# Performance work log

Hardware: AMD Instinct MI355X
Metric: run time of the kernel (lower is better)

## Reference

```python
import jax, jax.numpy as jnp
import numpy as np

N = 100000   # atoms (nodes)
M = 1600000  # bonds (edges)
D = 64       # atom_fea_len


def setup_inputs() -> dict:
    key = jax.random.key(0)
    ks = jax.random.split(key, 8)
    atom_weights = jax.random.uniform(ks[0], (N, 1), dtype=jnp.float32)
    atom_in_fea = jax.random.normal(ks[1], (N, D), dtype=jnp.float32)
    self_fea_idx = jnp.sort(jax.random.randint(ks[2], (M,), 0, N))
    nbr_fea_idx = jax.random.randint(ks[3], (M,), 0, N)
    # message_nn: Linear(2D->D) + LeakyReLU + Linear(D->D)
    W1 = jax.random.normal(ks[4], (2 * D, D), dtype=jnp.float32) * (1.0 / np.sqrt(2 * D))
    b1 = jnp.zeros((D,), dtype=jnp.float32)
    W2 = jax.random.normal(ks[5], (D, D), dtype=jnp.float32) * (1.0 / np.sqrt(D))
    b2 = jnp.zeros((D,), dtype=jnp.float32)
    # pool_nn (gate): Linear(D->1)
    Wg = jax.random.normal(ks[6], (D, 1), dtype=jnp.float32) * (1.0 / np.sqrt(D))
    bg = jnp.zeros((1,), dtype=jnp.float32)
    return {"atom_weights": atom_weights, "atom_in_fea": atom_in_fea,
            "self_fea_idx": self_fea_idx, "nbr_fea_idx": nbr_fea_idx,
            "W1": W1, "b1": b1, "W2": W2, "b2": b2, "Wg": Wg, "bg": bg}


def reference(atom_weights, atom_in_fea, self_fea_idx, nbr_fea_idx,
              W1, b1, W2, b2, Wg, bg):
    n = atom_in_fea.shape[0]
    # gather-concat: [M, 2D]
    fea = jnp.concatenate([atom_in_fea[self_fea_idx], atom_in_fea[nbr_fea_idx]], axis=1)
    # message_nn MLP -> [M, D]
    fea = jax.nn.leaky_relu(fea @ W1 + b1) @ W2 + b2
    # weighted scatter-softmax attention pooling over segments self_fea_idx
    gate = fea @ Wg + bg                                    # [M, 1]
    gmax = jax.ops.segment_max(gate, self_fea_idx, num_segments=n)  # [N, 1]
    gate = jnp.exp(gate - gmax[self_fea_idx])
    gate = atom_weights[nbr_fea_idx] * gate                 # [M, 1]
    denom = jax.ops.segment_sum(gate, self_fea_idx, num_segments=n)  # [N, 1]
    gate = gate / (denom[self_fea_idx] + 1e-13)
    pooled = jax.ops.segment_sum(gate * fea, self_fea_idx, num_segments=n)  # [N, D]
    return pooled + atom_in_fea
```

## Files before the change

### kernel.cpp

```cpp
#include <hip/hip_runtime.h>
#include <math.h>

typedef float f32x4 __attribute__((ext_vector_type(4)));
typedef __bf16 bf16x8 __attribute__((ext_vector_type(8)));

__global__ void build_row_start(const int* __restrict__ self_idx,
                                int* __restrict__ row_start, int M, int N) {
  int i = blockIdx.x * blockDim.x + threadIdx.x;
  if (i >= M) return;
  int cur = self_idx[i];
  int prev = (i == 0) ? -1 : self_idx[i - 1];
  for (int j = prev + 1; j <= cur; ++j) row_start[j] = i;
  if (i == M - 1) {
    for (int j = cur + 1; j <= N; ++j) row_start[j] = M;
  }
}

__global__ __launch_bounds__(256, 2)
void precompute_uy(const float* __restrict__ atom_fea,
                   const float* __restrict__ W1,
                   const float* __restrict__ b1,
                   const float* __restrict__ W2,
                   __bf16* __restrict__ Ub, __bf16* __restrict__ Yb,
                   __bf16* __restrict__ W2pack, int N) {
  const int lane = threadIdx.x & 63;
  const int r16 = lane & 15, g = lane >> 4;
  const int wid = (blockIdx.x * blockDim.x + threadIdx.x) >> 6;
  const int nw = (gridDim.x * blockDim.x) >> 6;

  if (wid == 0) {
#pragma unroll
    for (int ks = 0; ks < 2; ++ks)
#pragma unroll
      for (int c = 0; c < 4; ++c) {
        bf16x8 t;
#pragma unroll
        for (int jj = 0; jj < 8; ++jj)
          t[jj] = (__bf16)W2[(size_t)(32 * ks + 8 * g + jj) * 64 + 16 * c + r16];
        *(bf16x8*)(W2pack + ((size_t)(ks * 4 + c) * 64 + lane) * 8) = t;
      }
  }

  bf16x8 wt[2][4], wb[2][4];
#pragma unroll
  for (int ks = 0; ks < 2; ++ks)
#pragma unroll
    for (int c = 0; c < 4; ++c) {
      bf16x8 t, b;
#pragma unroll
      for (int jj = 0; jj < 8; ++jj) {
        int k = 32 * ks + 8 * g + jj;
        t[jj] = (__bf16)W1[(size_t)k * 64 + 16 * c + r16];
        b[jj] = (__bf16)W1[(size_t)(64 + k) * 64 + 16 * c + r16];
      }
      wt[ks][c] = t; wb[ks][c] = b;
    }
  float b1c[4];
#pragma unroll
  for (int c = 0; c < 4; ++c) b1c[c] = b1[16 * c + r16];

  const int nTiles = (N + 15) >> 4;
  for (int tile = wid; tile < nTiles; tile += nw) {
    const int a0 = tile * 16;
    int arow = a0 + r16; if (arow >= N) arow = N - 1;

    bf16x8 af[2];
#pragma unroll
    for (int ks = 0; ks < 2; ++ks) {
      const float* p = atom_fea + (size_t)arow * 64 + 32 * ks + 8 * g;
      f32x4 x0 = *(const f32x4*)p;
      f32x4 x1 = *(const f32x4*)(p + 4);
      bf16x8 a;
#pragma unroll
      for (int jj = 0; jj < 4; ++jj) { a[jj] = (__bf16)x0[jj]; a[4 + jj] = (__bf16)x1[jj]; }
      af[ks] = a;
    }

    f32x4 uacc[4], yacc[4];
#pragma unroll
    for (int c = 0; c < 4; ++c) { uacc[c] = (f32x4)0.0f; yacc[c] = (f32x4)0.0f; }
#pragma unroll
    for (int ks = 0; ks < 2; ++ks)
#pragma unroll
      for (int c = 0; c < 4; ++c) {
        uacc[c] = __builtin_amdgcn_mfma_f32_16x16x32_bf16(af[ks], wt[ks][c], uacc[c], 0, 0, 0);
        yacc[c] = __builtin_amdgcn_mfma_f32_16x16x32_bf16(af[ks], wb[ks][c], yacc[c], 0, 0, 0);
      }

#pragma unroll
    for (int c = 0; c < 4; ++c)
#pragma unroll
      for (int j = 0; j < 4; ++j) {
        int row = a0 + 4 * g + j;
        if (row < N) {
          Ub[(size_t)row * 64 + 16 * c + r16] = (__bf16)(uacc[c][j] + b1c[c]);
          Yb[(size_t)row * 64 + 16 * c + r16] = (__bf16)yacc[c][j];
        }
      }
  }
}

__global__ __launch_bounds__(64, 4)
void fused_pool(const float* __restrict__ atom_w,
                const float* __restrict__ atom_fea,
                const int* __restrict__ nbr_idx,
                const float* __restrict__ W2,
                const float* __restrict__ b2,
                const float* __restrict__ Wg,
                const float* __restrict__ bg,
                const int* __restrict__ row_start,
                const __bf16* __restrict__ Ub,
                const __bf16* __restrict__ Yb,
                const __bf16* __restrict__ W2pack,
                float* __restrict__ out, int N) {
  const int lane = threadIdx.x & 63;
  const int r16 = lane & 15, g = lane >> 4;
  const int wid = blockIdx.x;
  const int nw = gridDim.x;

  float wgl = 0.f;
  {
    const float* w2row = W2 + (size_t)lane * 64;
#pragma unroll
    for (int d = 0; d < 64; ++d) wgl = fmaf(w2row[d], Wg[d], wgl);
  }
  float wgsl[16];
#pragma unroll
  for (int ks = 0; ks < 2; ++ks)
#pragma unroll
    for (int jj = 0; jj < 8; ++jj)
      wgsl[ks * 8 + jj] = __shfl(wgl, 32 * ks + 8 * g + jj);

  float tb = b2[lane] * Wg[lane];
#pragma unroll
  for (int off = 1; off < 64; off <<= 1) tb += __shfl_xor(tb, off);
  const float bgp = bg[0] + tb;
  const float b2l = b2[lane];

  int s = wid;
  int nStart = 0, nEnd = 0;
  bf16x8 nu0 = {}, nu1 = {};
  if (s < N) {
    nStart = row_start[s];
    nEnd = row_start[s + 1];
    nu0 = *(const bf16x8*)(Ub + (size_t)s * 64 + 8 * g);
    nu1 = *(const bf16x8*)(Ub + (size_t)s * 64 + 32 + 8 * g);
  }

  for (; s < N; s += nw) {
    const int start = nStart, end = nEnd;
    const bf16x8 u0 = nu0, u1 = nu1;
    const float xr = atom_fea[(size_t)s * 64 + lane];

    const int s2 = s + nw;
    if (s2 < N) {
      nStart = row_start[s2];
      nEnd = row_start[s2 + 1];
      nu0 = *(const bf16x8*)(Ub + (size_t)s2 * 64 + 8 * g);
      nu1 = *(const bf16x8*)(Ub + (size_t)s2 * 64 + 32 + 8 * g);
    }

    float uf[16];
#pragma unroll
    for (int jj = 0; jj < 8; ++jj) {
      uf[jj] = (float)u0[jj];
      uf[8 + jj] = (float)u1[jj];
    }

    float zacc[16];
#pragma unroll
    for (int k = 0; k < 16; ++k) zacc[k] = 0.f;
    float wsum = 0.f;

    for (int base = start; base < end; base += 16) {
      const int er = base + r16;
      const bool valid = er < end;
      const int nb = valid ? nbr_idx[er] : 0;
      const float aw = atom_w[nb];
      const __bf16* yrow = Yb + ((size_t)nb << 6);
      const bf16x8 y0 = *(const bf16x8*)(yrow + 8 * g);
      const bf16x8 y1 = *(const bf16x8*)(yrow + 32 + 8 * g);

      float hf[16];
#pragma unroll
      for (int jj = 0; jj < 8; ++jj) {
        float a = uf[jj] + (float)y0[jj];
        float b = uf[8 + jj] + (float)y1[jj];
        hf[jj] = fmaxf(a, 0.01f * a);
        hf[8 + jj] = fmaxf(b, 0.01f * b);
      }

      float p0 = 0.f, p1 = 0.f;
#pragma unroll
      for (int i = 0; i < 8; ++i) {
        p0 = fmaf(hf[i], wgsl[i], p0);
        p1 = fmaf(hf[8 + i], wgsl[8 + i], p1);
      }
      float p = p0 + p1;
      p += __shfl_xor(p, 16);
      p += __shfl_xor(p, 32);

      const float w = valid ? aw * __expf(p + bgp) : 0.f;
      wsum += w;
#pragma unroll
      for (int k = 0; k < 16; ++k) zacc[k] = fmaf(w, hf[k], zacc[k]);
    }

    bf16x8 zf0, zf1;
#pragma unroll
    for (int jj = 0; jj < 8; ++jj) {
      zf0[jj] = (__bf16)zacc[jj];
      zf1[jj] = (__bf16)zacc[8 + jj];
    }

    f32x4 facc[4];
#pragma unroll
    for (int c = 0; c < 4; ++c) facc[c] = (f32x4)0.0f;
#pragma unroll
    for (int c = 0; c < 4; ++c) {
      const bf16x8 wf0 = *(const bf16x8*)(W2pack + ((size_t)(0 * 4 + c) * 64 + lane) * 8);
      const bf16x8 wf1 = *(const bf16x8*)(W2pack + ((size_t)(1 * 4 + c) * 64 + lane) * 8);
      facc[c] = __builtin_amdgcn_mfma_f32_16x16x32_bf16(zf0, wf0, facc[c], 0, 0, 0);
      facc[c] = __builtin_amdgcn_mfma_f32_16x16x32_bf16(zf1, wf1, facc[c], 0, 0, 0);
    }

    float accv[4];
#pragma unroll
    for (int c = 0; c < 4; ++c) {
      float a = (facc[c][0] + facc[c][1]) + (facc[c][2] + facc[c][3]);
      a += __shfl_xor(a, 16);
      a += __shfl_xor(a, 32);
      accv[c] = a;
    }

    float ssum = wsum;
    ssum += __shfl_xor(ssum, 1);
    ssum += __shfl_xor(ssum, 2);
    ssum += __shfl_xor(ssum, 4);
    ssum += __shfl_xor(ssum, 8);

    float val = accv[0];
    val = (g == 1) ? accv[1] : val;
    val = (g == 2) ? accv[2] : val;
    val = (g == 3) ? accv[3] : val;
    val = fmaf(ssum, b2l, val);

    out[(size_t)s * 64 + lane] = val / (ssum + 1e-13f) + xr;
  }
}

extern "C" void kernel_launch(void* const* d_in, const int* in_sizes, int n_in,
                              void* d_out, int out_size, void* d_ws, size_t ws_size,
                              hipStream_t stream) {
  const float* atom_w   = (const float*)d_in[0];
  const float* atom_fea = (const float*)d_in[1];
  const int*   self_idx = (const int*)d_in[2];
  const int*   nbr_idx  = (const int*)d_in[3];
  const float* W1 = (const float*)d_in[4];
  const float* b1 = (const float*)d_in[5];
  const float* W2 = (const float*)d_in[6];
  const float* b2 = (const float*)d_in[7];
  const float* Wg = (const float*)d_in[8];
  const float* bg = (const float*)d_in[9];
  float* out = (float*)d_out;

  const int N = in_sizes[0];
  const int M = in_sizes[2];

  char* ws = (char*)d_ws;
  int* row_start = (int*)ws;
  size_t off = ((size_t)(N + 1) * sizeof(int) + 255) & ~(size_t)255;
  __bf16* W2pack = (__bf16*)(ws + off);
  __bf16* Ub = W2pack + 8 * 64 * 8;
  __bf16* Yb = Ub + (size_t)N * 64;

  hipLaunchKernelGGL(build_row_start, dim3((M + 255) / 256), dim3(256), 0,
                     stream, self_idx, row_start, M, N);
  hipLaunchKernelGGL(precompute_uy, dim3(512), dim3(256), 0, stream,
                     atom_fea, W1, b1, W2, Ub, Yb, W2pack, N);
  hipLaunchKernelGGL(fused_pool, dim3(8192), dim3(64), 0, stream,
                     atom_w, atom_fea, nbr_idx, W2, b2, Wg, bg,
                     row_start, Ub, Yb, W2pack, out, N);
}
```

Baseline: 107.5 us.

## Process two atoms per wave with interleaved edge gathers in fused_pool

Each wave in the fused pooling kernel now handles a pair of consecutive atoms, issuing the neighbor gathers for both atoms before computing either one. The aim is more independent memory requests in flight per wave to hide gather latency, and to amortize the W2 MFMA epilogue over two atoms. The cross-iteration prefetch of row_start and U is removed, and launch bounds drop from 4 to 3 to make room for the extra registers. That lowers occupancy, and pairs with unequal degree leave one half idle.

Result: slower. 122.2 us (+13.7%).

```diff
diff --git a/kernel.cpp b/kernel.cpp
--- a/kernel.cpp
+++ b/kernel.cpp
@@ -100,7 +100,7 @@
   }
 }
 
-__global__ __launch_bounds__(64, 4)
+__global__ __launch_bounds__(64, 3)
 void fused_pool(const float* __restrict__ atom_w,
                 const float* __restrict__ atom_fea,
                 const int* __restrict__ nbr_idx,
@@ -115,8 +115,6 @@
                 float* __restrict__ out, int N) {
   const int lane = threadIdx.x & 63;
   const int r16 = lane & 15, g = lane >> 4;
-  const int wid = blockIdx.x;
-  const int nw = gridDim.x;
 
   float wgl = 0.f;
   {
@@ -137,115 +135,158 @@
   const float bgp = bg[0] + tb;
   const float b2l = b2[lane];
 
-  int s = wid;
-  int nStart = 0, nEnd = 0;
-  bf16x8 nu0 = {}, nu1 = {};
-  if (s < N) {
-    nStart = row_start[s];
-    nEnd = row_start[s + 1];
-    nu0 = *(const bf16x8*)(Ub + (size_t)s * 64 + 8 * g);
-    nu1 = *(const bf16x8*)(Ub + (size_t)s * 64 + 32 + 8 * g);
-  }
-
-  for (; s < N; s += nw) {
-    const int start = nStart, end = nEnd;
-    const bf16x8 u0 = nu0, u1 = nu1;
-    const float xr = atom_fea[(size_t)s * 64 + lane];
-
-    const int s2 = s + nw;
-    if (s2 < N) {
-      nStart = row_start[s2];
-      nEnd = row_start[s2 + 1];
-      nu0 = *(const bf16x8*)(Ub + (size_t)s2 * 64 + 8 * g);
-      nu1 = *(const bf16x8*)(Ub + (size_t)s2 * 64 + 32 + 8 * g);
-    }
-
-    float uf[16];
+  const int pstride = 2 * gridDim.x;
+  for (int p0 = 2 * blockIdx.x; p0 < N; p0 += pstride) {
+    const int sA = p0;
+    const int sB = p0 + 1;
+    const bool hasB = sB < N;
+
+    const int startA = row_start[sA];
+    const int endA = row_start[sA + 1];
+    const int startB = hasB ? row_start[sB] : 0;
+    const int endB = hasB ? row_start[sB + 1] : 0;
+
+    float ufA[16], ufB[16];
+    {
+      const bf16x8 a0 = *(const bf16x8*)(Ub + (size_t)sA * 64 + 8 * g);
+      const bf16x8 a1 = *(const bf16x8*)(Ub + (size_t)sA * 64 + 32 + 8 * g);
+      const bf16x8 c0 = hasB ? *(const bf16x8*)(Ub + (size_t)sB * 64 + 8 * g) : a0;
+      const bf16x8 c1 = hasB ? *(const bf16x8*)(Ub + (size_t)sB * 64 + 32 + 8 * g) : a1;
+#pragma unroll
+      for (int jj = 0; jj < 8; ++jj) {
+        ufA[jj] = (float)a0[jj]; ufA[8 + jj] = (float)a1[jj];
+        ufB[jj] = (float)c0[jj]; ufB[8 + jj] = (float)c1[jj];
+      }
+    }
+
+    float zA[16], zB[16];
+#pragma unroll
+    for (int k = 0; k < 16; ++k) { zA[k] = 0.f; zB[k] = 0.f; }
+    float wsumA = 0.f, wsumB = 0.f;
+
+    const int nTA = (endA - startA + 15) >> 4;
+    const int nTB = (endB - startB + 15) >> 4;
+    const int nT = nTA > nTB ? nTA : nTB;
+
+    for (int t = 0; t < nT; ++t) {
+      const int baseA = startA + 16 * t;
+      const int baseB = startB + 16 * t;
+      const bool actA = baseA < endA;
+      const bool actB = hasB && baseB < endB;
+
+      int nbA = 0; bf16x8 yA0 = {}, yA1 = {}; float awA = 0.f; bool vA = false;
+      int nbB = 0; bf16x8 yB0 = {}, yB1 = {}; float awB = 0.f; bool vB = false;
+      if (actA) {
+        const int e = baseA + r16; vA = e < endA;
+        nbA = vA ? nbr_idx[e] : 0;
+        const __bf16* yr = Yb + ((size_t)nbA << 6);
+        yA0 = *(const bf16x8*)(yr + 8 * g);
+        yA1 = *(const bf16x8*)(yr + 32 + 8 * g);
+        awA = atom_w[nbA];
+      }
+      if (actB) {
+        const int e = baseB + r16; vB = e < endB;
+        nbB = vB ? nbr_idx[e] : 0;
+        const __bf16* yr = Yb + ((size_t)nbB << 6);
+        yB0 = *(const bf16x8*)(yr + 8 * g);
+        yB1 = *(const bf16x8*)(yr + 32 + 8 * g);
+        awB = atom_w[nbB];
+      }
+
+      if (actA) {
+        float hf[16];
+#pragma unroll
+        for (int jj = 0; jj < 8; ++jj) {
+          float a = ufA[jj] + (float)yA0[jj];
+          float b = ufA[8 + jj] + (float)yA1[jj];
+          hf[jj] = fmaxf(a, 0.01f * a);
+          hf[8 + jj] = fmaxf(b, 0.01f * b);
+        }
+        float pacc = 0.f;
+#pragma unroll
+        for (int i = 0; i < 16; ++i) pacc = fmaf(hf[i], wgsl[i], pacc);
+        pacc += __shfl_xor(pacc, 16);
+        pacc += __shfl_xor(pacc, 32);
+        const float w = vA ? awA * __expf(pacc + bgp) : 0.f;
+        wsumA += w;
+#pragma unroll
+        for (int k = 0; k < 16; ++k) zA[k] = fmaf(w, hf[k], zA[k]);
+      }
+      if (actB) {
+        float hf[16];
+#pragma unroll
+        for (int jj = 0; jj < 8; ++jj) {
+          float a = ufB[jj] + (float)yB0[jj];
+          float b = ufB[8 + jj] + (float)yB1[jj];
+          hf[jj] = fmaxf(a, 0.01f * a);
+          hf[8 + jj] = fmaxf(b, 0.01f * b);
+        }
+        float pacc = 0.f;
+#pragma unroll
+        for (int i = 0; i < 16; ++i) pacc = fmaf(hf[i], wgsl[i], pacc);
+        pacc += __shfl_xor(pacc, 16);
+        pacc += __shfl_xor(pacc, 32);
+        const float w = vB ? awB * __expf(pacc + bgp) : 0.f;
+        wsumB += w;
+#pragma unroll
+        for (int k = 0; k < 16; ++k) zB[k] = fmaf(w, hf[k], zB[k]);
+      }
+    }
+
+    const float xrA = atom_fea[(size_t)sA * 64 + lane];
+    const float xrB = hasB ? atom_fea[(size_t)sB * 64 + lane] : 0.f;
+
+    bf16x8 zfA0, zfA1, zfB0, zfB1;
 #pragma unroll
     for (int jj = 0; jj < 8; ++jj) {
-      uf[jj] = (float)u0[jj];
-      uf[8 + jj] = (float)u1[jj];
-    }
-
-    float zacc[16];
-#pragma unroll
-    for (int k = 0; k < 16; ++k) zacc[k] = 0.f;
-    float wsum = 0.f;
-
-    for (int base = start; base < end; base += 16) {
-      const int er = base + r16;
-      const bool valid = er < end;
-      const int nb = valid ? nbr_idx[er] : 0;
-      const float aw = atom_w[nb];
-      const __bf16* yrow = Yb + ((size_t)nb << 6);
-      const bf16x8 y0 = *(const bf16x8*)(yrow + 8 * g);
-      const bf16x8 y1 = *(const bf16x8*)(yrow + 32 + 8 * g);
-
-      float hf[16];
-#pragma unroll
-      for (int jj = 0; jj < 8; ++jj) {
-        float a = uf[jj] + (float)y0[jj];
-        float b = uf[8 + jj] + (float)y1[jj];
-        hf[jj] = fmaxf(a, 0.01f * a);
-        hf[8 + jj] = fmaxf(b, 0.01f * b);
-      }
-
-      float p0 = 0.f, p1 = 0.f;
-#pragma unroll
-      for (int i = 0; i < 8; ++i) {
-        p0 = fmaf(hf[i], wgsl[i], p0);
-        p1 = fmaf(hf[8 + i], wgsl[8 + i], p1);
-      }
-      float p = p0 + p1;
-      p += __shfl_xor(p, 16);
-      p += __shfl_xor(p, 32);
-
-      const float w = valid ? aw * __expf(p + bgp) : 0.f;
-      wsum += w;
-#pragma unroll
-      for (int k = 0; k < 16; ++k) zacc[k] = fmaf(w, hf[k], zacc[k]);
-    }
-
-    bf16x8 zf0, zf1;
-#pragma unroll
-    for (int jj = 0; jj < 8; ++jj) {
-      zf0[jj] = (__bf16)zacc[jj];
-      zf1[jj] = (__bf16)zacc[8 + jj];
-    }
-
-    f32x4 facc[4];
-#pragma unroll
-    for (int c = 0; c < 4; ++c) facc[c] = (f32x4)0.0f;
+      zfA0[jj] = (__bf16)zA[jj]; zfA1[jj] = (__bf16)zA[8 + jj];
+      zfB0[jj] = (__bf16)zB[jj]; zfB1[jj] = (__bf16)zB[8 + jj];
+    }
+
+    f32x4 fA[4], fB[4];
+#pragma unroll
+    for (int c = 0; c < 4; ++c) { fA[c] = (f32x4)0.0f; fB[c] = (f32x4)0.0f; }
 #pragma unroll
     for (int c = 0; c < 4; ++c) {
       const bf16x8 wf0 = *(const bf16x8*)(W2pack + ((size_t)(0 * 4 + c) * 64 + lane) * 8);
       const bf16x8 wf1 = *(const bf16x8*)(W2pack + ((size_t)(1 * 4 + c) * 64 + lane) * 8);
-      facc[c] = __builtin_amdgcn_mfma_f32_16x16x32_bf16(zf0, wf0, facc[c], 0, 0, 0);
-      facc[c] = __builtin_amdgcn_mfma_f32_16x16x32_bf16(zf1, wf1, facc[c], 0, 0, 0);
-    }
-
-    float accv[4];
+      fA[c] = __builtin_amdgcn_mfma_f32_16x16x32_bf16(zfA0, wf0, fA[c], 0, 0, 0);
+      fA[c] = __builtin_amdgcn_mfma_f32_16x16x32_bf16(zfA1, wf1, fA[c], 0, 0, 0);
+      fB[c] = __builtin_amdgcn_mfma_f32_16x16x32_bf16(zfB0, wf0, fB[c], 0, 0, 0);
+      fB[c] = __builtin_amdgcn_mfma_f32_16x16x32_bf16(zfB1, wf1, fB[c], 0, 0, 0);
+    }
+
+    float avA[4], avB[4];
 #pragma unroll
     for (int c = 0; c < 4; ++c) {
-      float a = (facc[c][0] + facc[c][1]) + (facc[c][2] + facc[c][3]);
-      a += __shfl_xor(a, 16);
-      a += __shfl_xor(a, 32);
-      accv[c] = a;
-    }
-
-    float ssum = wsum;
-    ssum += __shfl_xor(ssum, 1);
-    ssum += __shfl_xor(ssum, 2);
-    ssum += __shfl_xor(ssum, 4);
-    ssum += __shfl_xor(ssum, 8);
-
-    float val = accv[0];
-    val = (g == 1) ? accv[1] : val;
-    val = (g == 2) ? accv[2] : val;
-    val = (g == 3) ? accv[3] : val;
-    val = fmaf(ssum, b2l, val);
-
-    out[(size_t)s * 64 + lane] = val / (ssum + 1e-13f) + xr;
+      float a = (fA[c][0] + fA[c][1]) + (fA[c][2] + fA[c][3]);
+      float b = (fB[c][0] + fB[c][1]) + (fB[c][2] + fB[c][3]);
+      a += __shfl_xor(a, 16); b += __shfl_xor(b, 16);
+      a += __shfl_xor(a, 32); b += __shfl_xor(b, 32);
+      avA[c] = a; avB[c] = b;
+    }
+    float ssA = wsumA, ssB = wsumB;
+#pragma unroll
+    for (int off = 1; off < 16; off <<= 1) {
+      ssA += __shfl_xor(ssA, off);
+      ssB += __shfl_xor(ssB, off);
+    }
+
+    float valA = avA[0];
+    valA = (g == 1) ? avA[1] : valA;
+    valA = (g == 2) ? avA[2] : valA;
+    valA = (g == 3) ? avA[3] : valA;
+    valA = fmaf(ssA, b2l, valA);
+    out[(size_t)sA * 64 + lane] = valA / (ssA + 1e-13f) + xrA;
+
+    if (hasB) {
+      float valB = avB[0];
+      valB = (g == 1) ? avB[1] : valB;
+      valB = (g == 2) ? avB[2] : valB;
+      valB = (g == 3) ? avB[3] : valB;
+      valB = fmaf(ssB, b2l, valB);
+      out[(size_t)sB * 64 + lane] = valB / (ssB + 1e-13f) + xrB;
+    }
   }
 }
 
```

## Software-pipeline neighbor gathers across segments and pack bf16 math into float2

Applied to the files above, without the earlier changes.

Adds a multi-stage software pipeline to the per-atom loop. Row bounds are prefetched two atoms ahead, the first neighbor chunk's index, Y row and weight one atom ahead, and each next chunk's neighbor index one iteration ahead, so the dependent gather latency overlaps with compute. The bf16-to-float unpacking now uses bit shifts on packed u32 words, and the edge math is done as float2 vectors so the compiler can emit packed FP32 ops. In exchange it holds more live registers, which may cut occupancy, and the first-chunk and steady-state code paths are duplicated.

Measured after the change: 132.2 us. 23.0% more time.

```diff
diff --git a/kernel.cpp b/kernel.cpp
--- a/kernel.cpp
+++ b/kernel.cpp
@@ -2,7 +2,17 @@
 #include <math.h>
 
 typedef float f32x4 __attribute__((ext_vector_type(4)));
+typedef float f32x2 __attribute__((ext_vector_type(2)));
 typedef __bf16 bf16x8 __attribute__((ext_vector_type(8)));
+typedef unsigned int u32;
+typedef u32 u32x4 __attribute__((ext_vector_type(4)));
+
+__device__ __forceinline__ f32x2 bfpair(u32 u) {
+  f32x2 r;
+  r[0] = __builtin_bit_cast(float, u << 16);
+  r[1] = __builtin_bit_cast(float, u & 0xffff0000u);
+  return r;
+}
 
 __global__ void build_row_start(const int* __restrict__ self_idx,
                                 int* __restrict__ row_start, int M, int N) {
@@ -124,12 +134,15 @@
 #pragma unroll
     for (int d = 0; d < 64; ++d) wgl = fmaf(w2row[d], Wg[d], wgl);
   }
-  float wgsl[16];
-#pragma unroll
-  for (int ks = 0; ks < 2; ++ks)
-#pragma unroll
-    for (int jj = 0; jj < 8; ++jj)
-      wgsl[ks * 8 + jj] = __shfl(wgl, 32 * ks + 8 * g + jj);
+  f32x2 wg2p[8];
+#pragma unroll
+  for (int pI = 0; pI < 8; ++pI) {
+    const int ks = pI >> 2, jj = (pI & 3) * 2;
+    f32x2 t;
+    t[0] = __shfl(wgl, 32 * ks + 8 * g + jj);
+    t[1] = __shfl(wgl, 32 * ks + 8 * g + jj + 1);
+    wg2p[pI] = t;
+  }
 
   float tb = b2[lane] * Wg[lane];
 #pragma unroll
@@ -138,79 +151,122 @@
   const float b2l = b2[lane];
 
   int s = wid;
-  int nStart = 0, nEnd = 0;
-  bf16x8 nu0 = {}, nu1 = {};
-  if (s < N) {
-    nStart = row_start[s];
-    nEnd = row_start[s + 1];
-    nu0 = *(const bf16x8*)(Ub + (size_t)s * 64 + 8 * g);
-    nu1 = *(const bf16x8*)(Ub + (size_t)s * 64 + 32 + 8 * g);
+  if (s >= N) return;
+
+  int curS, curE;
+  int nxtS = 0, nxtE = 0;
+  int nnS = 0, nnE = 0;
+  u32x4 cu0, cu1; float cxr;
+  u32x4 nu0 = {}, nu1 = {}; float nxr = 0.f;
+  u32x4 fy0, fy1; float faw; bool fv;
+  u32x4 py0 = {}, py1 = {}; float paw = 0.f; bool pv = false; int pnb = 0;
+
+  curS = row_start[s]; curE = row_start[s + 1];
+  cu0 = *(const u32x4*)(Ub + (size_t)s * 64 + 8 * g);
+  cu1 = *(const u32x4*)(Ub + (size_t)s * 64 + 32 + 8 * g);
+  cxr = atom_fea[(size_t)s * 64 + lane];
+  {
+    const int e = curS + r16; fv = e < curE;
+    const int nb = fv ? nbr_idx[e] : 0;
+    fy0 = *(const u32x4*)(Yb + ((size_t)nb << 6) + 8 * g);
+    fy1 = *(const u32x4*)(Yb + ((size_t)nb << 6) + 32 + 8 * g);
+    faw = atom_w[nb];
+  }
+  if (s + nw < N) {
+    nxtS = row_start[s + nw]; nxtE = row_start[s + nw + 1];
+    nu0 = *(const u32x4*)(Ub + (size_t)(s + nw) * 64 + 8 * g);
+    nu1 = *(const u32x4*)(Ub + (size_t)(s + nw) * 64 + 32 + 8 * g);
+    nxr = atom_fea[(size_t)(s + nw) * 64 + lane];
   }
 
   for (; s < N; s += nw) {
-    const int start = nStart, end = nEnd;
-    const bf16x8 u0 = nu0, u1 = nu1;
-    const float xr = atom_fea[(size_t)s * 64 + lane];
-
-    const int s2 = s + nw;
-    if (s2 < N) {
-      nStart = row_start[s2];
-      nEnd = row_start[s2 + 1];
-      nu0 = *(const bf16x8*)(Ub + (size_t)s2 * 64 + 8 * g);
-      nu1 = *(const bf16x8*)(Ub + (size_t)s2 * 64 + 32 + 8 * g);
-    }
-
-    float uf[16];
-#pragma unroll
-    for (int jj = 0; jj < 8; ++jj) {
-      uf[jj] = (float)u0[jj];
-      uf[8 + jj] = (float)u1[jj];
-    }
-
-    float zacc[16];
-#pragma unroll
-    for (int k = 0; k < 16; ++k) zacc[k] = 0.f;
+    const int start = curS, end = curE;
+    const int s1 = s + nw, s2 = s + 2 * nw;
+
+    if (s2 < N) { nnS = row_start[s2]; nnE = row_start[s2 + 1]; }
+
+    if (s1 < N) {
+      const int e = nxtS + r16; pv = e < nxtE;
+      pnb = pv ? nbr_idx[e] : 0;
+    }
+    int nb1 = (start + 16 + r16 < end) ? nbr_idx[start + 16 + r16] : 0;
+
+    f32x2 uf2[8];
+#pragma unroll
+    for (int pI = 0; pI < 4; ++pI) {
+      uf2[pI] = bfpair(cu0[pI]);
+      uf2[4 + pI] = bfpair(cu1[pI]);
+    }
+
+    f32x2 z2[8];
+#pragma unroll
+    for (int k = 0; k < 8; ++k) z2[k] = (f32x2)0.0f;
     float wsum = 0.f;
 
-    for (int base = start; base < end; base += 16) {
-      const int er = base + r16;
-      const bool valid = er < end;
-      const int nb = valid ? nbr_idx[er] : 0;
-      const float aw = atom_w[nb];
-      const __bf16* yrow = Yb + ((size_t)nb << 6);
-      const bf16x8 y0 = *(const bf16x8*)(yrow + 8 * g);
-      const bf16x8 y1 = *(const bf16x8*)(yrow + 32 + 8 * g);
-
-      float hf[16];
-#pragma unroll
-      for (int jj = 0; jj < 8; ++jj) {
-        float a = uf[jj] + (float)y0[jj];
-        float b = uf[8 + jj] + (float)y1[jj];
-        hf[jj] = fmaxf(a, 0.01f * a);
-        hf[8 + jj] = fmaxf(b, 0.01f * b);
-      }
-
-      float p0 = 0.f, p1 = 0.f;
-#pragma unroll
-      for (int i = 0; i < 8; ++i) {
-        p0 = fmaf(hf[i], wgsl[i], p0);
-        p1 = fmaf(hf[8 + i], wgsl[8 + i], p1);
-      }
-      float p = p0 + p1;
+    {
+      f32x2 h2[8];
+      f32x2 d2 = (f32x2)0.0f;
+#pragma unroll
+      for (int pI = 0; pI < 8; ++pI) {
+        const u32 yw = (pI < 4) ? fy0[pI] : fy1[pI - 4];
+        f32x2 a = uf2[pI] + bfpair(yw);
+        f32x2 t = a * 0.01f;
+        f32x2 h; h[0] = fmaxf(a[0], t[0]); h[1] = fmaxf(a[1], t[1]);
+        h2[pI] = h;
+        d2 += h * wg2p[pI];
+      }
+      float p = d2[0] + d2[1];
       p += __shfl_xor(p, 16);
       p += __shfl_xor(p, 32);
-
-      const float w = valid ? aw * __expf(p + bgp) : 0.f;
+      const float w = fv ? faw * __expf(p + bgp) : 0.f;
       wsum += w;
-#pragma unroll
-      for (int k = 0; k < 16; ++k) zacc[k] = fmaf(w, hf[k], zacc[k]);
+      const f32x2 w2 = {w, w};
+#pragma unroll
+      for (int k = 0; k < 8; ++k) z2[k] += w2 * h2[k];
+    }
+
+    if (s1 < N) {
+      py0 = *(const u32x4*)(Yb + ((size_t)pnb << 6) + 8 * g);
+      py1 = *(const u32x4*)(Yb + ((size_t)pnb << 6) + 32 + 8 * g);
+      paw = atom_w[pnb];
+    }
+
+    for (int base = start + 16; base < end; base += 16) {
+      const bool v = base + r16 < end;
+      const int nb = nb1;
+      nb1 = (base + 16 + r16 < end) ? nbr_idx[base + 16 + r16] : 0;
+      const u32x4 y0 = *(const u32x4*)(Yb + ((size_t)nb << 6) + 8 * g);
+      const u32x4 y1 = *(const u32x4*)(Yb + ((size_t)nb << 6) + 32 + 8 * g);
+      const float aw = atom_w[nb];
+
+      f32x2 h2[8];
+      f32x2 d2 = (f32x2)0.0f;
+#pragma unroll
+      for (int pI = 0; pI < 8; ++pI) {
+        const u32 yw = (pI < 4) ? y0[pI] : y1[pI - 4];
+        f32x2 a = uf2[pI] + bfpair(yw);
+        f32x2 t = a * 0.01f;
+        f32x2 h; h[0] = fmaxf(a[0], t[0]); h[1] = fmaxf(a[1], t[1]);
+        h2[pI] = h;
+        d2 += h * wg2p[pI];
+      }
+      float p = d2[0] + d2[1];
+      p += __shfl_xor(p, 16);
+      p += __shfl_xor(p, 32);
+      const float w = v ? aw * __expf(p + bgp) : 0.f;
+      wsum += w;
+      const f32x2 w2 = {w, w};
+#pragma unroll
+      for (int k = 0; k < 8; ++k) z2[k] += w2 * h2[k];
     }
 
     bf16x8 zf0, zf1;
 #pragma unroll
-    for (int jj = 0; jj < 8; ++jj) {
-      zf0[jj] = (__bf16)zacc[jj];
-      zf1[jj] = (__bf16)zacc[8 + jj];
+    for (int pI = 0; pI < 4; ++pI) {
+      zf0[2 * pI] = (__bf16)z2[pI][0];
+      zf0[2 * pI + 1] = (__bf16)z2[pI][1];
+      zf1[2 * pI] = (__bf16)z2[4 + pI][0];
+      zf1[2 * pI + 1] = (__bf16)z2[4 + pI][1];
     }
 
     f32x4 facc[4];
@@ -232,7 +288,6 @@
       a += __shfl_xor(a, 32);
       accv[c] = a;
     }
-
     float ssum = wsum;
     ssum += __shfl_xor(ssum, 1);
     ssum += __shfl_xor(ssum, 2);
@@ -245,7 +300,17 @@
     val = (g == 3) ? accv[3] : val;
     val = fmaf(ssum, b2l, val);
 
-    out[(size_t)s * 64 + lane] = val / (ssum + 1e-13f) + xr;
+    out[(size_t)s * 64 + lane] = val / (ssum + 1e-13f) + cxr;
+
+    curS = nxtS; curE = nxtE;
+    cu0 = nu0; cu1 = nu1; cxr = nxr;
+    nxtS = nnS; nxtE = nnE;
+    if (s2 < N) {
+      nu0 = *(const u32x4*)(Ub + (size_t)s2 * 64 + 8 * g);
+      nu1 = *(const u32x4*)(Ub + (size_t)s2 * 64 + 32 + 8 * g);
+      nxr = atom_fea[(size_t)s2 * 64 + lane];
+    }
+    fy0 = py0; fy1 = py1; faw = paw; fv = pv;
   }
 }
 
```
